# Performance work log

Measured on AMD Instinct MI355X. Metric: run time of the kernel, lower is better.

The kernel has to match this reference:

```python
import jax, jax.numpy as jnp
import numpy as np


def setup_inputs() -> dict:
    key = jax.random.key(0)
    ks = jax.random.split(key, 6)
    B, Nab, Nag, d, K = 16, 16384, 16384, 128, 10
    return {
        "H1": jax.random.normal(ks[0], (B, Nab, d), jnp.float32),
        "H2": jax.random.normal(ks[1], (B, Nag, d), jnp.float32),
        "X1": jax.random.normal(ks[2], (B, Nab, 3), jnp.float32),
        "X2": jax.random.normal(ks[3], (B, Nag, 3), jnp.float32),
        "W1": jax.random.uniform(ks[4], (K, d, d), jnp.float32),
        "W2": jax.random.uniform(ks[5], (K, d, d), jnp.float32),
    }


def _kabsch(P, Q):
    # Rigid alignment: find R (3x3), t (3,) s.t. P @ R + t ~= Q (least squares).
    c1 = P.mean(axis=0)
    c2 = Q.mean(axis=0)
    Pc = P - c1
    Qc = Q - c2
    Hm = Pc.T @ Qc  # [3,3] covariance
    U, S, Vt = jnp.linalg.svd(Hm, full_matrices=False)
    sign = jnp.sign(jnp.linalg.det(U @ Vt))
    Dm = jnp.diag(jnp.concatenate([jnp.ones(2, dtype=P.dtype), sign[None]]))
    R = U @ Dm @ Vt
    t = c2 - c1 @ R
    return P @ R + t, R, t


def reference(H1, H2, X1, X2, W1, W2):
    # Keypoint cross-attention. Faithful to torch:
    #   alpha_1k = softmax( (H1 @ W1_k @ H2.T).mean(dim=1) / sqrt(d) )
    # Using mean-over-columns identity: (H1 @ W @ H2.T).mean(1) = H1 @ W @ mean(H2,0)
    d = H1.shape[-1]
    scale = 1.0 / np.sqrt(d)
    h2bar = H2.mean(axis=1)  # [B, d]
    h1bar = H1.mean(axis=1)  # [B, d]
    v1 = jnp.einsum('kde,be->bkd', W1, h2bar)          # W1_k @ mean(H2)
    s1 = jnp.einsum('bnd,bkd->bkn', H1, v1) * scale     # [B, K, Nab]
    a1 = jax.nn.softmax(s1, axis=-1)
    Y1 = jnp.einsum('bkn,bnc->bkc', a1, X1)             # [B, K, 3]
    v2 = jnp.einsum('kde,be->bkd', W2, h1bar)
    s2 = jnp.einsum('bmd,bkd->bkm', H2, v2) * scale     # [B, K, Nag]
    a2 = jax.nn.softmax(s2, axis=-1)
    Y2 = jnp.einsum('bkm,bmc->bkc', a2, X2)             # [B, K, 3]
    Y1_aligned, R, t = jax.vmap(_kabsch)(Y1, Y2)
    return jnp.stack([Y1, Y2, Y1_aligned], axis=1)      # [B, 3, K, 3]
```

## Files before the change

### kernel.cpp

```cpp
#include <hip/hip_runtime.h>
#include <math.h>

#define NB 16
#define NN 16384
#define DD 128
#define KK 10
#define NT 128


__device__ __forceinline__ float4 f4add(float4 a, float4 b) {
    return make_float4(a.x + b.x, a.y + b.y, a.z + b.z, a.w + b.w);
}

__device__ __forceinline__ float kreduce16(const float a[KK], int l) {
    const bool h8 = (l & 8) != 0;
    const bool h4 = (l & 4) != 0;
    const bool h2 = (l & 2) != 0;
    const bool h1 = (l & 1) != 0;
    float b[8];
#pragma unroll
    for (int i = 0; i < 8; ++i) {
        float hi = (i < 2) ? a[i + 8] : 0.f;
        float give = h8 ? a[i] : hi;
        float keep = h8 ? hi : a[i];
        b[i] = keep + __shfl_xor(give, 8);
    }
    float c[4];
#pragma unroll
    for (int i = 0; i < 4; ++i) {
        float give = h4 ? b[i] : b[i + 4];
        float keep = h4 ? b[i + 4] : b[i];
        c[i] = keep + __shfl_xor(give, 4);
    }
    float d2[2];
#pragma unroll
    for (int i = 0; i < 2; ++i) {
        float give = h2 ? c[i] : c[i + 2];
        float keep = h2 ? c[i + 2] : c[i];
        d2[i] = keep + __shfl_xor(give, 2);
    }
    float give = h1 ? d2[0] : d2[1];
    float keep = h1 ? d2[1] : d2[0];
    return keep + __shfl_xor(give, 1);
}

__global__ __launch_bounds__(256) void k_sum(const float* __restrict__ H,
                                             float* __restrict__ hpart) {
    int bi = blockIdx.x;
    int b = bi >> 7;
    int chunk = bi & 127;
    const float4* src4 = (const float4*)(H + ((size_t)b * NN + (size_t)chunk * 128) * DD);
    int tid = threadIdx.x;
    float4 x[16];
#pragma unroll
    for (int j = 0; j < 16; ++j) x[j] = src4[j * 256 + tid];
    float4 t0 = f4add(x[0], x[1]),   t1 = f4add(x[2], x[3]);
    float4 t2 = f4add(x[4], x[5]),   t3 = f4add(x[6], x[7]);
    float4 t4 = f4add(x[8], x[9]),   t5 = f4add(x[10], x[11]);
    float4 t6 = f4add(x[12], x[13]), t7 = f4add(x[14], x[15]);
    float4 s = f4add(f4add(f4add(t0, t1), f4add(t2, t3)),
                     f4add(f4add(t4, t5), f4add(t6, t7)));
    s.x += __shfl_xor(s.x, 32);
    s.y += __shfl_xor(s.y, 32);
    s.z += __shfl_xor(s.z, 32);
    s.w += __shfl_xor(s.w, 32);
    __shared__ float red[4][32][4];
    int wv = tid >> 6, lane = tid & 63;
    if (lane < 32) {
        red[wv][lane][0] = s.x; red[wv][lane][1] = s.y;
        red[wv][lane][2] = s.z; red[wv][lane][3] = s.w;
    }
    __syncthreads();
    if (tid < 32) {
        float t0s = 0.f, t1s = 0.f, t2s = 0.f, t3s = 0.f;
#pragma unroll
        for (int w = 0; w < 4; ++w) {
            t0s += red[w][tid][0]; t1s += red[w][tid][1];
            t2s += red[w][tid][2]; t3s += red[w][tid][3];
        }
        *(float4*)(hpart + ((size_t)b * NT + chunk) * DD + tid * 4)
            = make_float4(t0s, t1s, t2s, t3s);
    }
}

__global__ __launch_bounds__(128) void k_v(const float* __restrict__ W,
                                           const float* __restrict__ hpart,
                                           float* __restrict__ vdst) {
    int bi = blockIdx.x;
    int b = bi / 10;
    int k = bi % 10;
    const float* Wk = W + (size_t)k * DD * DD;
    __shared__ __align__(16) float hs[DD];
    int tid = threadIdx.x;
    const float* hp = hpart + (size_t)b * NT * DD + tid;
    float s = 0.f;
#pragma unroll 8
    for (int c = 0; c < NT; ++c) s += hp[(size_t)c * DD];
    hs[tid] = s;
    __syncthreads();
    const float4* Wrow = (const float4*)(Wk + (size_t)tid * DD);
    const float4* h4p = (const float4*)hs;
    float acc = 0.f;
#pragma unroll 8
    for (int e4 = 0; e4 < 32; ++e4) {
        float4 w4 = Wrow[e4];
        float4 h4 = h4p[e4];
        acc += w4.x * h4.x + w4.y * h4.y + w4.z * h4.z + w4.w * h4.w;
    }
    const float SCALE = (float)(1.0 / (16384.0 * 11.313708498984761));
    vdst[((size_t)b * KK + k) * DD + tid] = acc * SCALE;
}

template <bool FOLD>
__global__ __launch_bounds__(256) void k_scores(const float* __restrict__ Hsrc,
                                                const float* __restrict__ Xsrc,
                                                const float* __restrict__ vsrc,
                                                float* __restrict__ spartp,
                                                float* __restrict__ hpartdst) {
    int bi = blockIdx.x;
    int b = bi >> 7;
    int tile = bi & 127;
    int row0 = tile << 7;
    const float* Hb = Hsrc + (size_t)b * NN * DD;
    const float* Xb = Xsrc + (size_t)b * NN * 3;
    const float* vp = vsrc + (size_t)b * KK * DD;

    __shared__ float4 v_s4[KK * DD / 4];
    __shared__ float red[4][40];
    __shared__ float4 colred4[4][2][16];

    int tid = threadIdx.x;
    for (int i = tid; i < KK * DD / 4; i += 256)
        v_s4[i] = ((const float4*)vp)[i];
    __syncthreads();

    int g = tid >> 4;
    int l = tid & 15;
    float kmask = (l < KK) ? 1.f : 0.f;

    float pse = 0.f, py0 = 0.f, py1 = 0.f, py2 = 0.f;
    float4 cs0 = make_float4(0.f, 0.f, 0.f, 0.f);
    float4 cs1 = make_float4(0.f, 0.f, 0.f, 0.f);

    int n0 = row0 + g * 2;
    const float* hp = Hb + (size_t)n0 * DD + (l << 2);
    float4 h00 = *(const float4*)(hp);
    float4 h01 = *(const float4*)(hp + 64);
    float4 h10 = *(const float4*)(hp + DD);
    float4 h11 = *(const float4*)(hp + DD + 64);
    float xa0 = Xb[(size_t)n0 * 3 + 0];
    float xa1 = Xb[(size_t)n0 * 3 + 1];
    float xa2 = Xb[(size_t)n0 * 3 + 2];
    float xb0 = Xb[(size_t)n0 * 3 + 3];
    float xb1 = Xb[(size_t)n0 * 3 + 4];
    float xb2 = Xb[(size_t)n0 * 3 + 5];

#pragma unroll
    for (int sweep = 0; sweep < 4; ++sweep) {
        float4 p00, p01, p10, p11;
        float qa0, qa1, qa2, qb0, qb1, qb2;
        if (sweep < 3) {
            const float* hpn = hp + (size_t)(sweep + 1) * 32 * DD;
            p00 = *(const float4*)(hpn);
            p01 = *(const float4*)(hpn + 64);
            p10 = *(const float4*)(hpn + DD);
            p11 = *(const float4*)(hpn + DD + 64);
            size_t xn = (size_t)(n0 + (sweep + 1) * 32) * 3;
            qa0 = Xb[xn + 0]; qa1 = Xb[xn + 1]; qa2 = Xb[xn + 2];
            qb0 = Xb[xn + 3]; qb1 = Xb[xn + 4]; qb2 = Xb[xn + 5];
        }
        if (FOLD) {
            cs0 = f4add(cs0, f4add(h00, h10));
            cs1 = f4add(cs1, f4add(h01, h11));
        }
        float acc0[KK], acc1[KK];
#pragma unroll
        for (int k = 0; k < KK; ++k) {
            float4 v0 = v_s4[k * 32 + l];
            float4 v1 = v_s4[k * 32 + 16 + l];
            acc0[k] = h00.x * v0.x + h00.y * v0.y + h00.z * v0.z + h00.w * v0.w
                    + h01.x * v1.x + h01.y * v1.y + h01.z * v1.z + h01.w * v1.w;
            acc1[k] = h10.x * v0.x + h10.y * v0.y + h10.z * v0.z + h10.w * v0.w
                    + h11.x * v1.x + h11.y * v1.y + h11.z * v1.z + h11.w * v1.w;
        }
        float s0 = kreduce16(acc0, l);
        float s1 = kreduce16(acc1, l);
        float e0 = kmask * __expf(s0);
        float e1 = kmask * __expf(s1);
        pse += e0 + e1;
        py0 += e0 * xa0 + e1 * xb0;
        py1 += e0 * xa1 + e1 * xb1;
        py2 += e0 * xa2 + e1 * xb2;
        if (sweep < 3) {
            h00 = p00; h01 = p01; h10 = p10; h11 = p11;
            xa0 = qa0; xa1 = qa1; xa2 = qa2;
            xb0 = qb0; xb1 = qb1; xb2 = qb2;
        }
    }
    pse += __shfl_xor(pse, 16); pse += __shfl_xor(pse, 32);
    py0 += __shfl_xor(py0, 16); py0 += __shfl_xor(py0, 32);
    py1 += __shfl_xor(py1, 16); py1 += __shfl_xor(py1, 32);
    py2 += __shfl_xor(py2, 16); py2 += __shfl_xor(py2, 32);
    if (FOLD) {
        cs0.x += __shfl_xor(cs0.x, 16); cs0.x += __shfl_xor(cs0.x, 32);
        cs0.y += __shfl_xor(cs0.y, 16); cs0.y += __shfl_xor(cs0.y, 32);
        cs0.z += __shfl_xor(cs0.z, 16); cs0.z += __shfl_xor(cs0.z, 32);
        cs0.w += __shfl_xor(cs0.w, 16); cs0.w += __shfl_xor(cs0.w, 32);
        cs1.x += __shfl_xor(cs1.x, 16); cs1.x += __shfl_xor(cs1.x, 32);
        cs1.y += __shfl_xor(cs1.y, 16); cs1.y += __shfl_xor(cs1.y, 32);
        cs1.z += __shfl_xor(cs1.z, 16); cs1.z += __shfl_xor(cs1.z, 32);
        cs1.w += __shfl_xor(cs1.w, 16); cs1.w += __shfl_xor(cs1.w, 32);
    }
    int wv = tid >> 6, lane = tid & 63;
    if (lane < 16) {
        if (lane < KK) {
            red[wv][lane] = pse;
            red[wv][10 + lane] = py0;
            red[wv][20 + lane] = py1;
            red[wv][30 + lane] = py2;
        }
        if (FOLD) {
            colred4[wv][0][lane] = cs0;
            colred4[wv][1][lane] = cs1;
        }
    }
    __syncthreads();
    if (tid < 40) {
        float s = red[0][tid] + red[1][tid] + red[2][tid] + red[3][tid];
        spartp[((size_t)b * NT + tile) * 40 + tid] = s;
    }
    if (FOLD && tid < DD) {
        int j = tid >> 6, cc = tid & 63, ll = cc >> 2, c = cc & 3;
        float s = 0.f;
#pragma unroll
        for (int w = 0; w < 4; ++w) s += ((const float*)&colred4[w][j][ll])[c];
        hpartdst[((size_t)b * NT + tile) * DD + tid] = s;
    }
}

__global__ __launch_bounds__(128) void k_final(const float* __restrict__ spart,
                                               float* __restrict__ out) {
    int b = blockIdx.x;
    int tid = threadIdx.x;
    __shared__ float acc[2][40];
    if (tid < 80) {
        int p = tid / 40, j = tid % 40;
        const float* sp = spart + (size_t)(p * NB + b) * NT * 40 + j;
        float s = 0.f;
        for (int tile = 0; tile < NT; ++tile) s += sp[(size_t)tile * 40];
        acc[p][j] = s;
    }
    __syncthreads();
    __shared__ float Ys[2][KK][3];
    if (tid < 2 * KK * 3) {
        int p = tid / 30;
        int r = tid % 30;
        int k = r / 3;
        int c = r % 3;
        float val = acc[p][10 + c * 10 + k] / acc[p][k];
        Ys[p][k][c] = val;
        out[((size_t)(b * 3 + p) * KK + k) * 3 + c] = val;
    }
    __syncthreads();
    if (tid == 0) {
        double P[KK][3], Q[KK][3];
        double c1[3] = {0, 0, 0}, c2[3] = {0, 0, 0};
        for (int i = 0; i < KK; ++i)
            for (int c = 0; c < 3; ++c) {
                P[i][c] = (double)Ys[0][i][c];
                Q[i][c] = (double)Ys[1][i][c];
                c1[c] += P[i][c];
                c2[c] += Q[i][c];
            }
        for (int c = 0; c < 3; ++c) { c1[c] /= KK; c2[c] /= KK; }
        double A0[3][3];
        for (int a = 0; a < 3; ++a)
            for (int c = 0; c < 3; ++c) {
                double s = 0;
                for (int i = 0; i < KK; ++i) s += (P[i][a] - c1[a]) * (Q[i][c] - c2[c]);
                A0[a][c] = s;
            }
        double Bm[3][3], V[3][3];
        for (int a = 0; a < 3; ++a)
            for (int c = 0; c < 3; ++c) { Bm[a][c] = A0[a][c]; V[a][c] = (a == c) ? 1.0 : 0.0; }
        for (int sweep = 0; sweep < 16; ++sweep)
            for (int p = 0; p < 2; ++p)
                for (int q = p + 1; q < 3; ++q) {
                    double al = 0, be = 0, ga = 0;
                    for (int r = 0; r < 3; ++r) {
                        al += Bm[r][p] * Bm[r][p];
                        be += Bm[r][q] * Bm[r][q];
                        ga += Bm[r][p] * Bm[r][q];
                    }
                    if (fabs(ga) < 1e-300) continue;
                    double zeta = (be - al) / (2.0 * ga);
                    double t = copysign(1.0, zeta) / (fabs(zeta) + sqrt(1.0 + zeta * zeta));
                    double cs = 1.0 / sqrt(1.0 + t * t);
                    double sn = cs * t;
                    for (int r = 0; r < 3; ++r) {
                        double bp = Bm[r][p], bq = Bm[r][q];
                        Bm[r][p] = cs * bp - sn * bq;
                        Bm[r][q] = sn * bp + cs * bq;
                        double vp = V[r][p], vq = V[r][q];
                        V[r][p] = cs * vp - sn * vq;
                        V[r][q] = sn * vp + cs * vq;
                    }
                }
        double sig[3];
        for (int j = 0; j < 3; ++j) {
            sig[j] = sqrt(Bm[0][j] * Bm[0][j] + Bm[1][j] * Bm[1][j] + Bm[2][j] * Bm[2][j]);
            if (sig[j] < 1e-300) sig[j] = 1e-300;
        }
        int jmin = 0;
        if (sig[1] < sig[jmin]) jmin = 1;
        if (sig[2] < sig[jmin]) jmin = 2;
        double det = A0[0][0] * (A0[1][1] * A0[2][2] - A0[1][2] * A0[2][1])
                   - A0[0][1] * (A0[1][0] * A0[2][2] - A0[1][2] * A0[2][0])
                   + A0[0][2] * (A0[1][0] * A0[2][1] - A0[1][1] * A0[2][0]);
        double sgn = (det >= 0.0) ? 1.0 : -1.0;
        double R[3][3];
        for (int a = 0; a < 3; ++a)
            for (int c = 0; c < 3; ++c) {
                double s = 0;
                for (int j = 0; j < 3; ++j) {
                    double dj = (j == jmin) ? sgn : 1.0;
                    s += dj * (Bm[a][j] / sig[j]) * V[c][j];
                }
                R[a][c] = s;
            }
        for (int i = 0; i < KK; ++i)
            for (int c = 0; c < 3; ++c) {
                double s = c2[c];
                for (int a = 0; a < 3; ++a) s += (P[i][a] - c1[a]) * R[a][c];
                out[((size_t)(b * 3 + 2) * KK + i) * 3 + c] = (float)s;
            }
    }
}

extern "C" void kernel_launch(void* const* d_in, const int* in_sizes, int n_in,
                              void* d_out, int out_size, void* d_ws, size_t ws_size,
                              hipStream_t stream) {
    const float* H1 = (const float*)d_in[0];
    const float* H2 = (const float*)d_in[1];
    const float* X1 = (const float*)d_in[2];
    const float* X2 = (const float*)d_in[3];
    const float* W1 = (const float*)d_in[4];
    const float* W2 = (const float*)d_in[5];
    float* out = (float*)d_out;
    float* ws = (float*)d_ws;
    float* hpart2 = ws;
    float* hpart1 = ws + 262144;
    float* v1     = ws + 524288;
    float* v2     = ws + 544768;
    float* spart  = ws + 565248;
    float* sp1 = spart;
    float* sp2 = spart + (size_t)NB * NT * 40;

    hipLaunchKernelGGL(k_sum,            dim3(2048), dim3(256), 0, stream, H2, hpart2);
    hipLaunchKernelGGL(k_v,              dim3(160),  dim3(128), 0, stream, W1, hpart2, v1);
    hipLaunchKernelGGL((k_scores<true>), dim3(2048), dim3(256), 0, stream,
                       H1, X1, v1, sp1, hpart1);
    hipLaunchKernelGGL(k_v,              dim3(160),  dim3(128), 0, stream, W2, hpart1, v2);
    hipLaunchKernelGGL((k_scores<false>),dim3(2048), dim3(256), 0, stream,
                       H2, X2, v2, sp2, (float*)nullptr);
    hipLaunchKernelGGL(k_final,          dim3(16),   dim3(128), 0, stream, spart, out);
}
```

Before: 355.2 us.

## Stage H tiles through LDS with async global_load_lds double buffering

Replaces the direct register prefetch of H rows in the scores kernel with asynchronous global-to-LDS loads into two 32-row shared buffers. Each chunk's next tile is issued before the current one is computed, and a barrier ends each chunk. The aim is deeper memory-latency hiding in this bandwidth-bound streaming kernel. In exchange it adds 32KB of LDS per block, which may lower occupancy, plus extra barriers and an LDS round trip.

Measured after the change: 361.8 us. About the same (+1.9%).

```diff
diff --git a/kernel.cpp b/kernel.cpp
--- a/kernel.cpp
+++ b/kernel.cpp
@@ -10,6 +10,13 @@
 
 __device__ __forceinline__ float4 f4add(float4 a, float4 b) {
     return make_float4(a.x + b.x, a.y + b.y, a.z + b.z, a.w + b.w);
+}
+
+__device__ __forceinline__ void gload_lds16(const float* g, float* l) {
+    __builtin_amdgcn_global_load_lds(
+        (const __attribute__((address_space(1))) unsigned int*)g,
+        (__attribute__((address_space(3))) unsigned int*)l,
+        16, 0, 0);
 }
 
 __device__ __forceinline__ float kreduce16(const float a[KK], int l) {
@@ -125,14 +132,23 @@
     const float* Xb = Xsrc + (size_t)b * NN * 3;
     const float* vp = vsrc + (size_t)b * KK * DD;
 
+    __shared__ float hb0[32 * DD];
+    __shared__ float hb1[32 * DD];
     __shared__ float4 v_s4[KK * DD / 4];
     __shared__ float red[4][40];
     __shared__ float4 colred4[4][2][16];
 
     int tid = threadIdx.x;
+    int wv = tid >> 6, lane = tid & 63;
+
     for (int i = tid; i < KK * DD / 4; i += 256)
         v_s4[i] = ((const float4*)vp)[i];
-    __syncthreads();
+    {
+        const float* gsrc = Hb + (size_t)(row0 + 8 * wv) * DD + lane * 4;
+#pragma unroll
+        for (int j = 0; j < 4; ++j)
+            gload_lds16(gsrc + j * 256, hb0 + (8 * wv + 2 * j) * DD);
+    }
 
     int g = tid >> 4;
     int l = tid & 15;
@@ -143,11 +159,6 @@
     float4 cs1 = make_float4(0.f, 0.f, 0.f, 0.f);
 
     int n0 = row0 + g * 2;
-    const float* hp = Hb + (size_t)n0 * DD + (l << 2);
-    float4 h00 = *(const float4*)(hp);
-    float4 h01 = *(const float4*)(hp + 64);
-    float4 h10 = *(const float4*)(hp + DD);
-    float4 h11 = *(const float4*)(hp + DD + 64);
     float xa0 = Xb[(size_t)n0 * 3 + 0];
     float xa1 = Xb[(size_t)n0 * 3 + 1];
     float xa2 = Xb[(size_t)n0 * 3 + 2];
@@ -155,20 +166,27 @@
     float xb1 = Xb[(size_t)n0 * 3 + 4];
     float xb2 = Xb[(size_t)n0 * 3 + 5];
 
-#pragma unroll
-    for (int sweep = 0; sweep < 4; ++sweep) {
-        float4 p00, p01, p10, p11;
+    __syncthreads();
+
+#pragma unroll
+    for (int c = 0; c < 4; ++c) {
+        const float* bufc = (c & 1) ? hb1 : hb0;
+        float* bufn = (c & 1) ? hb0 : hb1;
         float qa0, qa1, qa2, qb0, qb1, qb2;
-        if (sweep < 3) {
-            const float* hpn = hp + (size_t)(sweep + 1) * 32 * DD;
-            p00 = *(const float4*)(hpn);
-            p01 = *(const float4*)(hpn + 64);
-            p10 = *(const float4*)(hpn + DD);
-            p11 = *(const float4*)(hpn + DD + 64);
-            size_t xn = (size_t)(n0 + (sweep + 1) * 32) * 3;
+        if (c < 3) {
+            const float* gsrc = Hb + (size_t)(row0 + (c + 1) * 32 + 8 * wv) * DD + lane * 4;
+#pragma unroll
+            for (int j = 0; j < 4; ++j)
+                gload_lds16(gsrc + j * 256, bufn + (8 * wv + 2 * j) * DD);
+            size_t xn = (size_t)(n0 + (c + 1) * 32) * 3;
             qa0 = Xb[xn + 0]; qa1 = Xb[xn + 1]; qa2 = Xb[xn + 2];
             qb0 = Xb[xn + 3]; qb1 = Xb[xn + 4]; qb2 = Xb[xn + 5];
         }
+        const float* hp0 = bufc + (2 * g) * DD + (l << 2);
+        float4 h00 = *(const float4*)(hp0);
+        float4 h01 = *(const float4*)(hp0 + 64);
+        float4 h10 = *(const float4*)(hp0 + DD);
+        float4 h11 = *(const float4*)(hp0 + DD + 64);
         if (FOLD) {
             cs0 = f4add(cs0, f4add(h00, h10));
             cs1 = f4add(cs1, f4add(h01, h11));
@@ -191,11 +209,11 @@
         py0 += e0 * xa0 + e1 * xb0;
         py1 += e0 * xa1 + e1 * xb1;
         py2 += e0 * xa2 + e1 * xb2;
-        if (sweep < 3) {
-            h00 = p00; h01 = p01; h10 = p10; h11 = p11;
+        if (c < 3) {
             xa0 = qa0; xa1 = qa1; xa2 = qa2;
             xb0 = qb0; xb1 = qb1; xb2 = qb2;
         }
+        __syncthreads();
     }
     pse += __shfl_xor(pse, 16); pse += __shfl_xor(pse, 32);
     py0 += __shfl_xor(py0, 16); py0 += __shfl_xor(py0, 32);
@@ -211,7 +229,6 @@
         cs1.z += __shfl_xor(cs1.z, 16); cs1.z += __shfl_xor(cs1.z, 32);
         cs1.w += __shfl_xor(cs1.w, 16); cs1.w += __shfl_xor(cs1.w, 32);
     }
-    int wv = tid >> 6, lane = tid & 63;
     if (lane < 16) {
         if (lane < KK) {
             red[wv][lane] = pse;
```
